# Kernel optimization log

Measured on AMD Instinct MI355X. Metric: run time of the kernel, lower is better.

The kernel has to match this reference:

```python
import jax, jax.numpy as jnp
import numpy as np
import math

D_MODEL = 1024
N_HEADS = 16
HEAD_DIM = D_MODEL // N_HEADS  # 64
B, T = 2, 2048


def _rotate_half(x):
    x1, x2 = jnp.split(x, 2, axis=-1)
    return jnp.concatenate([-x2, x1], axis=-1)


def _rope_sin_cos(seq_len, dim, dtype=jnp.float32):
    # matches RotaryEmbedding: inv_freq over even indices, emb = [freqs, freqs]
    inv_freq = 1.0 / (10000.0 ** (jnp.arange(0, dim, 2, dtype=dtype) / dim))
    t = jnp.arange(seq_len, dtype=dtype)
    freqs = jnp.einsum('i,j->ij', t, inv_freq)          # [T, dim/2]
    emb = jnp.concatenate((freqs, freqs), axis=-1)      # [T, dim]
    sin = jnp.sin(emb)[None, :, None, :]                # [1, T, 1, dim]
    cos = jnp.cos(emb)[None, :, None, :]
    return sin, cos


def setup_inputs() -> dict:
    key = jax.random.key(0)
    k1, k2, k3 = jax.random.split(key, 3)
    x = jax.random.normal(k1, (B, T, D_MODEL), dtype=jnp.float32)
    # causal mask broadcast over batch and heads: [1, 1, T, T]
    mask = jnp.tril(jnp.ones((T, T), dtype=bool))[None, None]
    w_qkv = jax.random.normal(k2, (D_MODEL, 3 * D_MODEL), dtype=jnp.float32) / math.sqrt(D_MODEL)
    w_out = jax.random.normal(k3, (D_MODEL, D_MODEL), dtype=jnp.float32) / math.sqrt(D_MODEL)
    return {"x": x, "mask": mask, "w_qkv": w_qkv, "w_out": w_out}


def reference(x, mask, w_qkv, w_out):
    Bx, Tx, Dx = x.shape
    qkv = x @ w_qkv                                     # [B, T, 3D]
    q, k, v = jnp.split(qkv, 3, axis=-1)
    q = q.reshape(Bx, Tx, N_HEADS, HEAD_DIM)
    k = k.reshape(Bx, Tx, N_HEADS, HEAD_DIM)
    v = v.reshape(Bx, Tx, N_HEADS, HEAD_DIM)
    sin, cos = _rope_sin_cos(Tx, HEAD_DIM, x.dtype)
    q = q * cos + _rotate_half(q) * sin
    k = k * cos + _rotate_half(k) * sin
    scores = jnp.einsum('bthd,bThd->bhtT', q, k) / math.sqrt(HEAD_DIM)
    scores = jnp.where(mask, scores, -1e10)
    probs = jax.nn.softmax(scores, axis=-1)             # [B, H, T, T]
    out = jnp.einsum('bhtT,bThd->bthd', probs, v)
    out = out.reshape(Bx, Tx, Dx)
    return out @ w_out
```

## Files before the change

kernel.cpp:

```cpp
#include <hip/hip_runtime.h>
#include <math.h>

typedef unsigned short u16;
typedef __attribute__((ext_vector_type(8))) short short8;
typedef __attribute__((ext_vector_type(4))) float f32x4;

__device__ __forceinline__ u16 f2bf(float f) {
  unsigned int u = __float_as_uint(f);
  u += 0x7fffu + ((u >> 16) & 1u);
  return (u16)(u >> 16);
}
__device__ __forceinline__ float bf2f(u16 h) {
  return __uint_as_float(((unsigned int)h) << 16);
}

__device__ __forceinline__ f32x4 mfma16(short8 a, short8 b, f32x4 c) {
  return __builtin_amdgcn_mfma_f32_16x16x32_bf16(a, b, c, 0, 0, 0);
}

#define NEG_BIG (-1e30f)

__device__ __forceinline__ void glds16(const u16* g, u16* l) {
  __builtin_amdgcn_global_load_lds(
      (const __attribute__((address_space(1))) unsigned int*)g,
      (__attribute__((address_space(3))) unsigned int*)l, 16, 0, 0);
}

__global__ __launch_bounds__(256) void detect_dtype3(const u16* __restrict__ a,
                                                     const u16* __restrict__ bb,
                                                     const u16* __restrict__ c,
                                                     int* __restrict__ flags) {
  const u16* x = (blockIdx.x == 0) ? a : (blockIdx.x == 1) ? bb : c;
  __shared__ int cnt;
  if (threadIdx.x == 0) cnt = 0;
  __syncthreads();
  int my = 0;
  for (int i = threadIdx.x; i < 4096; i += 256) {
    float v = bf2f(x[2 * i]);
    float av = fabsf(v);
    if (v == 0.0f || (av >= 1e-4f && av <= 100.0f)) my++;
  }
  atomicAdd(&cnt, my);
  __syncthreads();
  if (threadIdx.x == 0) flags[blockIdx.x] = (cnt > 2458) ? 1 : 0;
}

__global__ __launch_bounds__(256) void prep_all(const void* __restrict__ wqkv,
                                                const void* __restrict__ wout,
                                                const void* __restrict__ xin,
                                                u16* __restrict__ wqkvT,
                                                u16* __restrict__ woutT,
                                                u16* __restrict__ xb,
                                                float2* __restrict__ tab,
                                                const int* __restrict__ flags) {
  int z = blockIdx.z;
  int tid = threadIdx.x;
  if (z == 2) {
    if (blockIdx.x >= 16 || blockIdx.y >= 16) return;
    int idx = (blockIdx.y * 16 + blockIdx.x) * 256 + tid;
    int t = idx >> 5, d = idx & 31;
    float invf = expf(-(float)d * 0.28782313662425575f);
    float s, c;
    sincosf((float)t * invf, &s, &c);
    tab[idx] = make_float2(c, s);
    return;
  }
  if (z == 3) {
    bool isbf = (flags[0] != 0);
    int tg = (blockIdx.y * 48 + blockIdx.x) * 256 + tid;
    for (int i = tg; i < 524288; i += 196608) {
      int base = i * 8;
      if (isbf) {
        *(short8*)(xb + base) = *(const short8*)((const u16*)xin + base);
      } else {
        const float* xf = (const float*)xin;
        f32x4 x0 = *(const f32x4*)(xf + base);
        f32x4 x1 = *(const f32x4*)(xf + base + 4);
        short8 o;
#pragma unroll
        for (int u = 0; u < 4; ++u) { o[u] = (short)f2bf(x0[u]); o[u + 4] = (short)f2bf(x1[u]); }
        *(short8*)(xb + base) = o;
      }
    }
    return;
  }
  const void* in = (z == 0) ? wqkv : wout;
  u16* out = (z == 0) ? wqkvT : woutT;
  int C = (z == 0) ? 3072 : 1024;
  const int R = 1024;
  bool isbf = (flags[z + 1] != 0);
  if (z == 1 && blockIdx.x >= 16) return;
  __shared__ float tile[64][68];
  int tc = blockIdx.x * 64, tr = blockIdx.y * 64;
  int r = tid >> 3, cg = (tid & 7) << 3;
#pragma unroll
  for (int p = 0; p < 2; ++p) {
    int row = r + p * 32;
    if (isbf) {
      short8 v = *(const short8*)((const u16*)in + (size_t)(tr + row) * C + tc + cg);
#pragma unroll
      for (int u = 0; u < 8; ++u) tile[row][cg + u] = bf2f((u16)v[u]);
    } else {
      const float* inf = (const float*)in + (size_t)(tr + row) * C + tc + cg;
#pragma unroll
      for (int u = 0; u < 8; ++u) tile[row][cg + u] = inf[u];
    }
  }
  __syncthreads();
#pragma unroll
  for (int p = 0; p < 2; ++p) {
    int orow = r + p * 32;
    short8 v;
#pragma unroll
    for (int u = 0; u < 8; ++u) v[u] = (short)f2bf(tile[cg + u][orow]);
    *(short8*)(out + (size_t)(tc + orow) * R + tr + cg) = v;
  }
}

__device__ __forceinline__ void qkv_epilogue3(f32x4 acc[4][4], int bm, int bn,
                                              int wm, int wn, int quad, int lane15,
                                              int lane, const float2* __restrict__ tab,
                                              u16* Qo, u16* Ko, u16* VTo, u16* myE) {
  int nbase = bn + wn * 64;
  int h = (nbase & 1023) >> 6;
  if (nbase < 2048) {
    int l8 = lane15 & 7, lh = lane15 >> 3;
#pragma unroll
    for (int i = 0; i < 4; ++i) {
#pragma unroll
      for (int r = 0; r < 4; ++r) {
        int mloc = i * 16 + quad * 4 + r;
        int t = (bm + wm * 64 + mloc) & 2047;
        float2 cs0 = tab[t * 32 + lane15];
        float2 cs1 = tab[t * 32 + 16 + lane15];
        float v0 = acc[i][0][r], v1 = acc[i][1][r], v2 = acc[i][2][r], v3 = acc[i][3][r];
        int m7 = mloc & 7;
        u16* rowp = myE + mloc * 64 + l8;
        rowp[((0 + lh) ^ m7) * 8] = f2bf(v0 * cs0.x - v2 * cs0.y);
        rowp[((2 + lh) ^ m7) * 8] = f2bf(v1 * cs1.x - v3 * cs1.y);
        rowp[((4 + lh) ^ m7) * 8] = f2bf(v2 * cs0.x + v0 * cs0.y);
        rowp[((6 + lh) ^ m7) * 8] = f2bf(v3 * cs1.x + v1 * cs1.y);
      }
    }
    asm volatile("s_waitcnt lgkmcnt(0)" ::: "memory");
    u16* dst = (nbase < 1024) ? Qo : Ko;
#pragma unroll
    for (int p = 0; p < 8; ++p) {
      int f = p * 64 + lane;
      int mr = f >> 3, nc = f & 7;
      short8 val = *(const short8*)(myE + mr * 64 + (nc ^ (mr & 7)) * 8);
      int g = bm + wm * 64 + mr;
      int bI = g >> 11, tI = g & 2047;
      *(short8*)(dst + ((size_t)(bI * 16 + h) * 2048 + tI) * 64 + nc * 8) = val;
    }
  } else {
#pragma unroll
    for (int i = 0; i < 4; ++i)
#pragma unroll
      for (int j = 0; j < 4; ++j)
#pragma unroll
        for (int r = 0; r < 4; ++r) {
          int col = i * 16 + quad * 4 + r;
          int slot = (col >> 3) ^ (lane15 & 7);
          myE[(j * 16 + lane15) * 64 + slot * 8 + (col & 7)] = f2bf(acc[i][j][r]);
        }
    asm volatile("s_waitcnt lgkmcnt(0)" ::: "memory");
    int g0 = bm + wm * 64;
    int bI = g0 >> 11, t0 = g0 & 2047;
#pragma unroll
    for (int p = 0; p < 8; ++p) {
      int f = p * 64 + lane;
      int dr = f >> 3, tc = f & 7;
      short8 val = *(const short8*)(myE + dr * 64 + (tc ^ (dr & 7)) * 8);
      *(short8*)(VTo + ((size_t)(bI * 16 + h) * 64 + dr) * 2048 + t0 + tc * 8) = val;
    }
  }
}

__global__ __launch_bounds__(256) void gemm_qkv_fast(const u16* __restrict__ X,
                                                     const u16* __restrict__ WT,
                                                     const float2* __restrict__ tab,
                                                     u16* __restrict__ Qo,
                                                     u16* __restrict__ Ko,
                                                     u16* __restrict__ VTo) {
  const int K = 1024;
  __shared__ u16 buf[16384];
  u16* lA = buf;
  u16* lB = buf + 8192;
  int tid = threadIdx.x;
  int wave = tid >> 6, lane = tid & 63;
  int lane15 = lane & 15, quad = lane >> 4;
  int wm = wave >> 1, wn = wave & 1;
  int bm = blockIdx.x * 128, bn = blockIdx.y * 128;
  f32x4 acc[4][4] = {};
  for (int k0 = 0; k0 < K; k0 += 64) {
    __syncthreads();
#pragma unroll
    for (int p = 0; p < 4; ++p) {
      int g = p * 4 + wave;
      int f = g * 64 + lane;
      int r = f >> 3;
      int c8 = (f & 7) ^ (r & 7);
      glds16(X + (size_t)(bm + r) * K + k0 + c8 * 8, lA + g * 512);
      glds16(WT + (size_t)(bn + r) * K + k0 + c8 * 8, lB + g * 512);
    }
    __syncthreads();
#pragma unroll
    for (int ks = 0; ks < 2; ++ks) {
      int so = ((ks * 4 + quad) ^ (lane15 & 7)) * 8;
      short8 af[4], bf[4];
#pragma unroll
      for (int i = 0; i < 4; ++i)
        af[i] = *(const short8*)(lA + (wm * 64 + i * 16 + lane15) * 64 + so);
#pragma unroll
      for (int j = 0; j < 4; ++j)
        bf[j] = *(const short8*)(lB + (wn * 64 + j * 16 + lane15) * 64 + so);
#pragma unroll
      for (int i = 0; i < 4; ++i)
#pragma unroll
        for (int j = 0; j < 4; ++j)
          acc[i][j] = mfma16(af[i], bf[j], acc[i][j]);
    }
  }
  __syncthreads();
  qkv_epilogue3(acc, bm, bn, wm, wn, quad, lane15, lane, tab, Qo, Ko, VTo,
                buf + wave * 4096);
}

__global__ __launch_bounds__(256) void gemm_qkv_rope(const void* __restrict__ Xv,
                                                     const u16* __restrict__ WT,
                                                     const float2* __restrict__ tab,
                                                     u16* __restrict__ Qo,
                                                     u16* __restrict__ Ko,
                                                     u16* __restrict__ VTo,
                                                     const int* __restrict__ flag) {
  const int K = 1024;
  __shared__ u16 buf[16384];
  u16* lA = buf;
  u16* lB = buf + 5120;
  bool isbf = (*flag != 0);
  int tid = threadIdx.x;
  int wave = tid >> 6, lane = tid & 63;
  int lane15 = lane & 15, quad = lane >> 4;
  int wm = wave >> 1, wn = wave & 1;
  int bm = blockIdx.x * 128, bn = blockIdx.y * 128;
  int sr = tid >> 2, scg = (tid & 3) << 3;
  f32x4 acc[4][4] = {};
  for (int k0 = 0; k0 < K; k0 += 32) {
    __syncthreads();
#pragma unroll
    for (int p = 0; p < 2; ++p) {
      int row = sr + p * 64;
      if (isbf) {
        *(short8*)(lA + row * 40 + scg) =
            *(const short8*)((const u16*)Xv + (size_t)(bm + row) * K + k0 + scg);
      } else {
        const float* xf = (const float*)Xv + (size_t)(bm + row) * K + k0 + scg;
        f32x4 x0 = *(const f32x4*)(xf);
        f32x4 x1 = *(const f32x4*)(xf + 4);
        short8 o;
#pragma unroll
        for (int u = 0; u < 4; ++u) { o[u] = (short)f2bf(x0[u]); o[u + 4] = (short)f2bf(x1[u]); }
        *(short8*)(lA + row * 40 + scg) = o;
      }
      *(short8*)(lB + row * 40 + scg) = *(const short8*)(WT + (size_t)(bn + row) * K + k0 + scg);
    }
    __syncthreads();
    short8 af[4], bf[4];
#pragma unroll
    for (int i = 0; i < 4; ++i)
      af[i] = *(const short8*)(lA + (wm * 64 + i * 16 + lane15) * 40 + quad * 8);
#pragma unroll
    for (int j = 0; j < 4; ++j)
      bf[j] = *(const short8*)(lB + (wn * 64 + j * 16 + lane15) * 40 + quad * 8);
#pragma unroll
    for (int i = 0; i < 4; ++i)
#pragma unroll
      for (int j = 0; j < 4; ++j)
        acc[i][j] = mfma16(af[i], bf[j], acc[i][j]);
  }
  __syncthreads();
  qkv_epilogue3(acc, bm, bn, wm, wn, quad, lane15, lane, tab, Qo, Ko, VTo,
                buf + wave * 4096);
}

__device__ __forceinline__ short8 lds_frag(const u16* buf, int row, int chunk) {
  int s = chunk ^ (row & 7);
  return *(const short8*)(buf + row * 64 + s * 8);
}

__device__ __forceinline__ void stage_tile(const u16* gK, const u16* gV,
                                           u16* lK, u16* lV, int wave, int lane) {
#pragma unroll
  for (int p = 0; p < 2; ++p) {
    int f = (p * 4 + wave) * 64 + lane;
    int r = f >> 3;
    int c = (f & 7) ^ (r & 7);
    glds16(gK + (size_t)r * 64 + c * 8, lK + (p * 4 + wave) * 512);
    glds16(gV + (size_t)r * 2048 + c * 8, lV + (p * 4 + wave) * 512);
  }
}

__global__ __launch_bounds__(256, 4) void attn_fused(const u16* __restrict__ Q,
                                                     const u16* __restrict__ K,
                                                     const u16* __restrict__ VT,
                                                     u16* __restrict__ Ao) {
  int bx = blockIdx.x;
  int bh = bx & 31;
  int kp = bx >> 5;
  int m = kp & 7, n = kp >> 3;
  int qt = (n == 0) ? m : (n == 1) ? (15 - m) : (n == 2) ? (16 + m) : (31 - m);
  int b = bh >> 4, h = bh & 15;
  int tid = threadIdx.x, wave = tid >> 6, lane = tid & 63;
  int lane15 = lane & 15, quad = lane >> 4;
  int q0 = qt * 64 + wave * 16;
  const u16* Qb = Q + (size_t)bh * 2048 * 64;
  const u16* Kb = K + (size_t)bh * 2048 * 64;
  const u16* Vb = VT + (size_t)bh * 64 * 2048;

  __shared__ u16 Kl[2][64 * 64];
  __shared__ u16 Vl[2][64 * 64];
  __shared__ u16 lP[4][16 * 64];
  u16* myP = lP[wave];

  short8 qf0 = *(const short8*)(Qb + (size_t)(q0 + lane15) * 64 + quad * 8);
  short8 qf1 = *(const short8*)(Qb + (size_t)(q0 + lane15) * 64 + 32 + quad * 8);

  f32x4 Ov[4] = {};
  float tsum[4] = {0.f, 0.f, 0.f, 0.f};

  int ntiles = qt + 1;
  stage_tile(Kb, Vb, Kl[0], Vl[0], wave, lane);

  for (int kt = 0; kt < ntiles; ++kt) {
    int kbase = kt * 64;
    int cur = kt & 1;
    __syncthreads();
    if (kt + 1 < ntiles)
      stage_tile(Kb + (size_t)(kbase + 64) * 64, Vb + kbase + 64,
                 Kl[cur ^ 1], Vl[cur ^ 1], wave, lane);

    f32x4 S[4];
#pragma unroll
    for (int j = 0; j < 4; ++j) {
      short8 k0 = lds_frag(Kl[cur], j * 16 + lane15, quad);
      short8 k1 = lds_frag(Kl[cur], j * 16 + lane15, 4 + quad);
      f32x4 z = {};
      z = mfma16(qf0, k0, z);
      z = mfma16(qf1, k1, z);
      S[j] = z;
    }
    if (kt == qt) {
#pragma unroll
      for (int j = 0; j < 4; ++j) {
        int kpos = kbase + j * 16 + lane15;
#pragma unroll
        for (int r = 0; r < 4; ++r)
          if (kpos > q0 + quad * 4 + r) S[j][r] = NEG_BIG;
      }
    }
#pragma unroll
    for (int j = 0; j < 4; ++j)
#pragma unroll
      for (int r = 0; r < 4; ++r) {
        float p = __expf(fmaf(S[j][r], 0.125f, -8.0f));
        S[j][r] = p;
        tsum[r] += p;
      }
#pragma unroll
    for (int j = 0; j < 4; ++j)
#pragma unroll
      for (int r = 0; r < 4; ++r) {
        int lrow = quad * 4 + r;
        int slot = (j * 2 + (lane15 >> 3)) ^ (lrow & 7);
        myP[lrow * 64 + slot * 8 + (lane15 & 7)] = f2bf(S[j][r]);
      }
    asm volatile("s_waitcnt lgkmcnt(0)" ::: "memory");
    short8 pa0 = *(const short8*)(myP + lane15 * 64 + ((quad) ^ (lane15 & 7)) * 8);
    short8 pa1 = *(const short8*)(myP + lane15 * 64 + ((4 + quad) ^ (lane15 & 7)) * 8);
#pragma unroll
    for (int j = 0; j < 4; ++j) {
      short8 v0 = lds_frag(Vl[cur], j * 16 + lane15, quad);
      short8 v1 = lds_frag(Vl[cur], j * 16 + lane15, 4 + quad);
      Ov[j] = mfma16(pa0, v0, Ov[j]);
      Ov[j] = mfma16(pa1, v1, Ov[j]);
    }
  }
  float rl[4];
#pragma unroll
  for (int r = 0; r < 4; ++r) {
    float v = tsum[r];
    v += __shfl_xor(v, 1);
    v += __shfl_xor(v, 2);
    v += __shfl_xor(v, 4);
    v += __shfl_xor(v, 8);
    rl[r] = 1.f / v;
  }
#pragma unroll
  for (int j = 0; j < 4; ++j)
#pragma unroll
    for (int r = 0; r < 4; ++r) {
      int t = q0 + quad * 4 + r;
      Ao[(size_t)(b * 2048 + t) * 1024 + h * 64 + j * 16 + lane15] =
          f2bf(Ov[j][r] * rl[r]);
    }
}

__global__ __launch_bounds__(256) void gemm_out(const u16* __restrict__ A,
                                                const u16* __restrict__ WT,
                                                float* __restrict__ out) {
  const int K = 1024;
  __shared__ u16 lA[64 * 128];
  __shared__ u16 lB[128 * 128];
  int tid = threadIdx.x;
  int wave = tid >> 6, lane = tid & 63;
  int lane15 = lane & 15, quad = lane >> 4;
  int wm = wave >> 1, wn = wave & 1;
  int bm = blockIdx.x * 64, bn = blockIdx.y * 128;
  f32x4 acc[2][4] = {};
  for (int k0 = 0; k0 < K; k0 += 128) {
    __syncthreads();
#pragma unroll
    for (int p = 0; p < 4; ++p) {
      int g = p * 4 + wave;
      int f = g * 64 + lane;
      int r = f >> 4;
      int c16 = (f & 15) ^ (r & 15);
      glds16(A + (size_t)(bm + r) * K + k0 + c16 * 8, lA + g * 512);
    }
#pragma unroll
    for (int p = 0; p < 8; ++p) {
      int g = p * 4 + wave;
      int f = g * 64 + lane;
      int r = f >> 4;
      int c16 = (f & 15) ^ (r & 15);
      glds16(WT + (size_t)(bn + r) * K + k0 + c16 * 8, lB + g * 512);
    }
    __syncthreads();
#pragma unroll
    for (int ks = 0; ks < 4; ++ks) {
      int so = ((ks * 4 + quad) ^ lane15) * 8;
      short8 af[2], bf[4];
#pragma unroll
      for (int i = 0; i < 2; ++i)
        af[i] = *(const short8*)(lA + (wm * 32 + i * 16 + lane15) * 128 + so);
#pragma unroll
      for (int j = 0; j < 4; ++j)
        bf[j] = *(const short8*)(lB + (wn * 64 + j * 16 + lane15) * 128 + so);
#pragma unroll
      for (int i = 0; i < 2; ++i)
#pragma unroll
        for (int j = 0; j < 4; ++j)
          acc[i][j] = mfma16(af[i], bf[j], acc[i][j]);
    }
  }
#pragma unroll
  for (int i = 0; i < 2; ++i)
#pragma unroll
    for (int r = 0; r < 4; ++r) {
      int m = bm + wm * 32 + i * 16 + quad * 4 + r;
      size_t rowo = (size_t)m * 1024 + bn + wn * 64 + lane15;
      out[rowo] = acc[i][0][r];
      out[rowo + 16] = acc[i][1][r];
      out[rowo + 32] = acc[i][2][r];
      out[rowo + 48] = acc[i][3][r];
    }
}

__global__ void ws_sentinel(float* out, float val) {
  if (threadIdx.x == 0) out[1] = val;
}

extern "C" void kernel_launch(void* const* d_in, const int* in_sizes, int n_in,
                              void* d_out, int out_size, void* d_ws, size_t ws_size,
                              hipStream_t stream) {
  (void)out_size;
  const void* x = nullptr;
  const void* w_qkv = nullptr;
  const void* w_out = nullptr;
  for (int i = 0; i < n_in; ++i) {
    if (in_sizes[i] == 4194304 && !x) x = d_in[i];
    else if (in_sizes[i] == 3145728 && !w_qkv) w_qkv = d_in[i];
    else if (in_sizes[i] == 1048576 && !w_out) w_out = d_in[i];
  }
  float* out = (float*)d_out;

  const size_t EL_B = 32 + 4194304 + 1048576 + 3 * 4194304 + 262144;
  const size_t REQ_B = EL_B * 2;
  const size_t REQ_A = (EL_B + 4194304) * 2;
  if (ws_size < REQ_B) {
    ws_sentinel<<<1, 64, 0, stream>>>(out, 1.0e6f + 1000.0f * (float)(ws_size >> 20));
    return;
  }
  int* flags = (int*)d_ws;
  u16* base = (u16*)d_ws + 32;
  u16* wqkvT = base;
  u16* attnw = base;
  u16* woutT = base + 4194304;
  u16* Qw = woutT + 1048576;
  u16* Kw = Qw + 4194304;
  u16* VTw = Kw + 4194304;
  float2* tab = (float2*)(VTw + 4194304);
  u16* xb = VTw + 4194304 + 262144;

  detect_dtype3<<<3, 256, 0, stream>>>((const u16*)x, (const u16*)w_qkv,
                                       (const u16*)w_out, flags);
  if (ws_size >= REQ_A) {
    prep_all<<<dim3(48, 16, 4), 256, 0, stream>>>(w_qkv, w_out, x, wqkvT, woutT,
                                                  xb, tab, flags);
    gemm_qkv_fast<<<dim3(32, 24), 256, 0, stream>>>(xb, wqkvT, tab, Qw, Kw, VTw);
  } else {
    prep_all<<<dim3(48, 16, 3), 256, 0, stream>>>(w_qkv, w_out, x, wqkvT, woutT,
                                                  nullptr, tab, flags);
    gemm_qkv_rope<<<dim3(32, 24), 256, 0, stream>>>(x, wqkvT, tab, Qw, Kw, VTw, flags + 0);
  }
  attn_fused<<<1024, 256, 0, stream>>>(Qw, Kw, VTw, attnw);
  gemm_out<<<dim3(64, 8), 256, 0, stream>>>(attnw, woutT, out);
}
```

Before: 205.6 us.

## Replace QKV GEMM with 256x256 tiled double-buffered kernel

Replaces the 128x128 single-buffered QKV projection GEMM with a 256x256-tile kernel using 512 threads and double-buffered LDS staging via global_load_lds, so the next K-tile loads while the current one computes. It also adds block-index swizzling for L2 locality, setprio around MFMA bursts, and a rewritten fused RoPE/transposed-V epilogue sized for the larger tile. The aim is more data reuse per load and less exposed memory latency. In exchange it uses 128KB of LDS per block and launches only 192 blocks, which may underfill the GPU.

```diff
diff --git a/kernel.cpp b/kernel.cpp
--- a/kernel.cpp
+++ b/kernel.cpp
@@ -177,54 +177,135 @@
   }
 }
 
-__global__ __launch_bounds__(256) void gemm_qkv_fast(const u16* __restrict__ X,
-                                                     const u16* __restrict__ WT,
-                                                     const float2* __restrict__ tab,
-                                                     u16* __restrict__ Qo,
-                                                     u16* __restrict__ Ko,
-                                                     u16* __restrict__ VTo) {
+__device__ __forceinline__ void stage256(const u16* __restrict__ X,
+                                         const u16* __restrict__ WT,
+                                         u16* lAq, u16* lBq,
+                                         int bm, int bn, int k0, int tid) {
   const int K = 1024;
-  __shared__ u16 buf[16384];
-  u16* lA = buf;
-  u16* lB = buf + 8192;
+#pragma unroll
+  for (int p = 0; p < 4; ++p) {
+    int cid = p * 512 + tid;
+    int r = cid >> 3;
+    int cs = (cid & 7) ^ (r & 7);
+    int dst = (cid & ~63) * 8;
+    glds16(X + (size_t)(bm + r) * K + k0 + cs * 8, lAq + dst);
+    glds16(WT + (size_t)(bn + r) * K + k0 + cs * 8, lBq + dst);
+  }
+}
+
+__global__ __launch_bounds__(512, 2) void gemm_qkv_256(const u16* __restrict__ X,
+                                                       const u16* __restrict__ WT,
+                                                       const float2* __restrict__ tab,
+                                                       u16* __restrict__ Qo,
+                                                       u16* __restrict__ Ko,
+                                                       u16* __restrict__ VTo) {
+  __shared__ u16 sh[65536];
   int tid = threadIdx.x;
   int wave = tid >> 6, lane = tid & 63;
   int lane15 = lane & 15, quad = lane >> 4;
-  int wm = wave >> 1, wn = wave & 1;
-  int bm = blockIdx.x * 128, bn = blockIdx.y * 128;
-  f32x4 acc[4][4] = {};
-  for (int k0 = 0; k0 < K; k0 += 64) {
-    __syncthreads();
-#pragma unroll
-    for (int p = 0; p < 4; ++p) {
-      int g = p * 4 + wave;
-      int f = g * 64 + lane;
-      int r = f >> 3;
-      int c8 = (f & 7) ^ (r & 7);
-      glds16(X + (size_t)(bm + r) * K + k0 + c8 * 8, lA + g * 512);
-      glds16(WT + (size_t)(bn + r) * K + k0 + c8 * 8, lB + g * 512);
-    }
-    __syncthreads();
-#pragma unroll
-    for (int ks = 0; ks < 2; ++ks) {
-      int so = ((ks * 4 + quad) ^ (lane15 & 7)) * 8;
-      short8 af[4], bf[4];
-#pragma unroll
-      for (int i = 0; i < 4; ++i)
-        af[i] = *(const short8*)(lA + (wm * 64 + i * 16 + lane15) * 64 + so);
+  int wm = wave >> 2, wn = wave & 3;
+  int swz = (blockIdx.x & 7) * 24 + (blockIdx.x >> 3);
+  int bm = (swz / 12) * 256, bn = (swz % 12) * 256;
+  f32x4 acc[8][4] = {};
+
+  stage256(X, WT, sh, sh + 32768, bm, bn, 0, tid);
+  asm volatile("s_waitcnt vmcnt(0)\n\ts_barrier" ::: "memory");
+
+#pragma unroll 2
+  for (int kt = 0; kt < 16; ++kt) {
+    int q = kt & 1;
+    if (kt < 15)
+      stage256(X, WT, sh + (q ^ 1) * 16384, sh + 32768 + (q ^ 1) * 16384,
+               bm, bn, (kt + 1) * 64, tid);
+    const u16* lAq = sh + q * 16384;
+    const u16* lBq = sh + 32768 + q * 16384;
+    short8 bfr[2][4];
+#pragma unroll
+    for (int j = 0; j < 4; ++j) {
+      int row = wn * 64 + j * 16 + lane15;
+      int ro = row * 64, r7 = row & 7;
+      bfr[0][j] = *(const short8*)(lBq + ro + (quad ^ r7) * 8);
+      bfr[1][j] = *(const short8*)(lBq + ro + ((4 + quad) ^ r7) * 8);
+    }
+#pragma unroll
+    for (int qd = 0; qd < 4; ++qd) {
+      short8 afr[2][2];
+#pragma unroll
+      for (int i2 = 0; i2 < 2; ++i2) {
+        int row = wm * 128 + (qd * 2 + i2) * 16 + lane15;
+        int ro = row * 64, r7 = row & 7;
+        afr[i2][0] = *(const short8*)(lAq + ro + (quad ^ r7) * 8);
+        afr[i2][1] = *(const short8*)(lAq + ro + ((4 + quad) ^ r7) * 8);
+      }
+      __builtin_amdgcn_s_setprio(1);
+#pragma unroll
+      for (int ks = 0; ks < 2; ++ks)
+#pragma unroll
+        for (int i2 = 0; i2 < 2; ++i2)
+#pragma unroll
+          for (int j = 0; j < 4; ++j)
+            acc[qd * 2 + i2][j] = mfma16(afr[i2][ks], bfr[ks][j], acc[qd * 2 + i2][j]);
+      __builtin_amdgcn_s_setprio(0);
+    }
+    asm volatile("s_waitcnt vmcnt(0)\n\ts_barrier" ::: "memory");
+  }
+  __syncthreads();
+
+  u16* myE = sh + wave * 8192;
+  int nbase = bn + wn * 64;
+  int h = (nbase & 1023) >> 6;
+  if (nbase < 2048) {
+    int l8 = lane15 & 7, lh = lane15 >> 3;
+#pragma unroll
+    for (int i = 0; i < 8; ++i) {
+#pragma unroll
+      for (int r = 0; r < 4; ++r) {
+        int mloc = i * 16 + quad * 4 + r;
+        int t = (bm + wm * 128 + mloc) & 2047;
+        float2 cs0 = tab[t * 32 + lane15];
+        float2 cs1 = tab[t * 32 + 16 + lane15];
+        float v0 = acc[i][0][r], v1 = acc[i][1][r], v2 = acc[i][2][r], v3 = acc[i][3][r];
+        int m7 = mloc & 7;
+        u16* rowp = myE + mloc * 64 + l8;
+        rowp[((0 + lh) ^ m7) * 8] = f2bf(v0 * cs0.x - v2 * cs0.y);
+        rowp[((2 + lh) ^ m7) * 8] = f2bf(v1 * cs1.x - v3 * cs1.y);
+        rowp[((4 + lh) ^ m7) * 8] = f2bf(v2 * cs0.x + v0 * cs0.y);
+        rowp[((6 + lh) ^ m7) * 8] = f2bf(v3 * cs1.x + v1 * cs1.y);
+      }
+    }
+    asm volatile("s_waitcnt lgkmcnt(0)" ::: "memory");
+    u16* dst = (nbase < 1024) ? Qo : Ko;
+#pragma unroll
+    for (int p = 0; p < 16; ++p) {
+      int f = p * 64 + lane;
+      int mr = f >> 3, nc = f & 7;
+      short8 val = *(const short8*)(myE + mr * 64 + (nc ^ (mr & 7)) * 8);
+      int g = bm + wm * 128 + mr;
+      int bI = g >> 11, tI = g & 2047;
+      *(short8*)(dst + ((size_t)(bI * 16 + h) * 2048 + tI) * 64 + nc * 8) = val;
+    }
+  } else {
+#pragma unroll
+    for (int i = 0; i < 8; ++i)
 #pragma unroll
       for (int j = 0; j < 4; ++j)
-        bf[j] = *(const short8*)(lB + (wn * 64 + j * 16 + lane15) * 64 + so);
-#pragma unroll
-      for (int i = 0; i < 4; ++i)
-#pragma unroll
-        for (int j = 0; j < 4; ++j)
-          acc[i][j] = mfma16(af[i], bf[j], acc[i][j]);
-    }
-  }
-  __syncthreads();
-  qkv_epilogue3(acc, bm, bn, wm, wn, quad, lane15, lane, tab, Qo, Ko, VTo,
-                buf + wave * 4096);
+#pragma unroll
+        for (int r = 0; r < 4; ++r) {
+          int col = i * 16 + quad * 4 + r;
+          int slot = (col >> 3) ^ (lane15 & 7);
+          myE[(j * 16 + lane15) * 128 + slot * 8 + (col & 7)] = f2bf(acc[i][j][r]);
+        }
+    asm volatile("s_waitcnt lgkmcnt(0)" ::: "memory");
+    int g0 = bm + wm * 128;
+    int bI = g0 >> 11, t0 = g0 & 2047;
+#pragma unroll
+    for (int p = 0; p < 16; ++p) {
+      int f = p * 64 + lane;
+      int dr = f >> 4, tc = f & 15;
+      short8 val = *(const short8*)(myE + dr * 128 + (tc ^ (dr & 7)) * 8);
+      *(short8*)(VTo + ((size_t)(bI * 16 + h) * 64 + dr) * 2048 + t0 + tc * 8) = val;
+    }
+  }
 }
 
 __global__ __launch_bounds__(256) void gemm_qkv_rope(const void* __restrict__ Xv,
@@ -508,7 +589,7 @@
   if (ws_size >= REQ_A) {
     prep_all<<<dim3(48, 16, 4), 256, 0, stream>>>(w_qkv, w_out, x, wqkvT, woutT,
                                                   xb, tab, flags);
-    gemm_qkv_fast<<<dim3(32, 24), 256, 0, stream>>>(xb, wqkvT, tab, Qw, Kw, VTw);
+    gemm_qkv_256<<<dim3(192), dim3(512), 0, stream>>>(xb, wqkvT, tab, Qw, Kw, VTw);
   } else {
     prep_all<<<dim3(48, 16, 3), 256, 0, stream>>>(w_qkv, w_out, x, wqkvT, woutT,
                                                   nullptr, tab, flags);
```

Result: faster. 191.0 us (-7.1%).
